# Kernel tuning notes

Hardware: AMD Instinct MI355X
Metric: run time of the kernel (lower is better)

## Reference

```python
import jax, jax.numpy as jnp
import numpy as np

B, P, M, C = 64, 8732, 16, 81
THRESHOLD = 0.5
NEG_POS_RATIO = 3
ALPHA = 1.0  # config.reg_weights
EPS = 1e-7


def cxcy_to_xy(c):
    return jnp.concatenate([c[..., :2] - c[..., 2:] / 2.0,
                            c[..., :2] + c[..., 2:] / 2.0], axis=-1)


def _rand_boxes_cxcy(key, shape):
    k1, k2 = jax.random.split(key)
    cxcy = jax.random.uniform(k1, shape + (2,), minval=0.2, maxval=0.8)
    wh = jax.random.uniform(k2, shape + (2,), minval=0.05, maxval=0.35)
    return jnp.concatenate([cxcy, wh], axis=-1)


def setup_inputs() -> dict:
    key = jax.random.key(0)
    ks = jax.random.split(key, 5)
    predicted_locs = cxcy_to_xy(_rand_boxes_cxcy(ks[0], (B, P)))          # valid corner boxes
    predicted_scores = jax.random.normal(ks[1], (B, P, C), dtype=jnp.float32)
    boxes = jnp.clip(cxcy_to_xy(_rand_boxes_cxcy(ks[2], (B, M))), 0.0, 1.0)  # GT corner boxes
    labels = jax.random.randint(ks[3], (B, M), 1, C)                       # object labels (1..C-1)
    priors_cxcy = _rand_boxes_cxcy(ks[4], (P,))
    return {"predicted_locs": predicted_locs, "predicted_scores": predicted_scores,
            "boxes": boxes, "labels": labels, "priors_cxcy": priors_cxcy}


def jaccard(a, b):
    # a: [M,4], b: [P,4] corner boxes -> [M,P] IoU
    lt = jnp.maximum(a[:, None, :2], b[None, :, :2])
    rb = jnp.minimum(a[:, None, 2:], b[None, :, 2:])
    wh = jnp.clip(rb - lt, 0.0)
    inter = wh[..., 0] * wh[..., 1]
    area_a = (a[:, 2] - a[:, 0]) * (a[:, 3] - a[:, 1])
    area_b = (b[:, 2] - b[:, 0]) * (b[:, 3] - b[:, 1])
    return inter / (area_a[:, None] + area_b[None, :] - inter)


def diou_loss(b1, b2):
    # corner boxes, elementwise over leading dims -> per-box loss 1 - DIoU
    lt = jnp.maximum(b1[..., :2], b2[..., :2])
    rb = jnp.minimum(b1[..., 2:], b2[..., 2:])
    wh = jnp.clip(rb - lt, 0.0)
    inter = wh[..., 0] * wh[..., 1]
    area1 = (b1[..., 2] - b1[..., 0]) * (b1[..., 3] - b1[..., 1])
    area2 = (b2[..., 2] - b2[..., 0]) * (b2[..., 3] - b2[..., 1])
    iou = inter / (area1 + area2 - inter + EPS)
    c1 = (b1[..., :2] + b1[..., 2:]) / 2.0
    c2 = (b2[..., :2] + b2[..., 2:]) / 2.0
    inter_diag = jnp.sum((c1 - c2) ** 2, axis=-1)
    enc_lt = jnp.minimum(b1[..., :2], b2[..., :2])
    enc_rb = jnp.maximum(b1[..., 2:], b2[..., 2:])
    outer_diag = jnp.sum((enc_rb - enc_lt) ** 2, axis=-1)
    dious = jnp.clip(iou - inter_diag / (outer_diag + EPS), -1.0, 1.0)
    return 1.0 - dious


def reference(predicted_locs, predicted_scores, boxes, labels, priors_cxcy):
    priors_xy = cxcy_to_xy(priors_cxcy)

    def assign(boxes_i, labels_i):
        overlap = jaccard(boxes_i, priors_xy)              # [M, P]
        ovl_prior = overlap.max(axis=0)                    # best overlap per prior
        obj_prior = overlap.argmax(axis=0)                 # best object per prior
        ovl_obj = overlap.max(axis=1)                      # best overlap per object
        prior_obj = overlap.argmax(axis=1)                 # best prior per object
        valid = ovl_obj > 0
        j_idx = jnp.cumsum(valid.astype(jnp.int32)) - 1    # index within filtered list (faithful)
        idx = jnp.where(valid, prior_obj, P)               # P -> dropped (out of bounds)
        ovl_prior = ovl_prior.at[idx].set(1.0, mode='drop')
        obj_prior = obj_prior.at[idx].set(j_idx, mode='drop')
        lab = labels_i[obj_prior]
        label_pos = jnp.where(ovl_prior < THRESHOLD, 0, lab)
        label_neg = jnp.where(ovl_prior < THRESHOLD - 0.1, -1, lab)
        return label_pos, label_neg

    true_classes, true_neg_classes = jax.vmap(assign)(boxes, labels)  # [B,P] each
    positive = true_classes > 0                                        # [B,P]
    pos_f = positive.astype(jnp.float32)
    n_pos_total = jnp.sum(pos_f)

    # Localization loss: DIoU(pred_pos, pred_pos) with reduce='mean' (faithful to source)
    per_box = diou_loss(predicted_locs, predicted_locs)                # [B,P]
    loc_loss = jnp.sum(per_box * pos_f) / jnp.maximum(n_pos_total, 1.0)

    # Confidence loss: per-prior CE + hard-negative mining (neg_pos_ratio)
    logp = jax.nn.log_softmax(predicted_scores, axis=-1)
    conf_all = -jnp.take_along_axis(logp, true_classes[..., None], axis=-1)[..., 0]  # [B,P]
    conf_pos_sum = jnp.sum(conf_all * pos_f)
    conf_neg = jnp.where(positive, 0.0, conf_all)
    conf_neg_sorted = -jnp.sort(-conf_neg, axis=-1)                    # descending
    n_hard = NEG_POS_RATIO * jnp.sum(positive, axis=1)                 # [B]
    hard_mask = (jnp.arange(P)[None, :] < n_hard[:, None]).astype(jnp.float32)
    conf_loss = (jnp.sum(conf_neg_sorted * hard_mask) + conf_pos_sum) / n_pos_total

    return conf_loss + ALPHA * loc_loss
```

## Files before the change

### kernel.cpp

```cpp
#include <hip/hip_runtime.h>
#include <math.h>

#define B_ 64
#define P_ 8732
#define M_ 16
#define C_ 81
#define THRESH 0.5f
#define EPS_ 1e-7f

#define CE_BLOCKS 2048
#define NBLK_CE CE_BLOCKS

__global__ __launch_bounds__(1024) void assign_kernel(
    const float* __restrict__ boxes,
    const int*   __restrict__ labels,
    const float* __restrict__ priors,
    int*         __restrict__ true_classes,
    int*         __restrict__ n_pos)
{
    const int b = blockIdx.x;
    const int tid = threadIdx.x;
    const int lane = tid & 63;
    const int wv = tid >> 6;

    __shared__ float s_ovl[P_];
    __shared__ unsigned char s_obj[P_];
    __shared__ float s_bx[M_][4];
    __shared__ float s_barea[M_];
    __shared__ int   s_lab[M_];
    __shared__ float s_wv[M_][16];
    __shared__ int   s_wp[M_][16];
    __shared__ float s_ovl_obj[M_];
    __shared__ int   s_prior_obj[M_];
    __shared__ int   s_cnt[16];

    if (tid < M_*4) ((float*)s_bx)[tid] = boxes[b*M_*4 + tid];
    if (tid < M_)   s_lab[tid] = labels[b*M_ + tid];
    __syncthreads();
    if (tid < M_)
        s_barea[tid] = (s_bx[tid][2]-s_bx[tid][0])*(s_bx[tid][3]-s_bx[tid][1]);
    __syncthreads();

    float bestv[M_]; int bestp[M_];
    #pragma unroll
    for (int m = 0; m < M_; ++m) { bestv[m] = -1.0f; bestp[m] = 0x7fffffff; }

    for (int p = tid; p < P_; p += 1024) {
        float4 pc = ((const float4*)priors)[p];
        float px1 = pc.x - pc.z*0.5f, py1 = pc.y - pc.w*0.5f;
        float px2 = pc.x + pc.z*0.5f, py2 = pc.y + pc.w*0.5f;
        float parea = (px2-px1)*(py2-py1);
        float bv = -1.0f; int bm = 0;
        #pragma unroll
        for (int m = 0; m < M_; ++m) {
            float ix1 = fmaxf(s_bx[m][0], px1);
            float iy1 = fmaxf(s_bx[m][1], py1);
            float ix2 = fminf(s_bx[m][2], px2);
            float iy2 = fminf(s_bx[m][3], py2);
            float iw = fmaxf(ix2-ix1, 0.0f);
            float ih = fmaxf(iy2-iy1, 0.0f);
            float inter = iw*ih;
            float iou = inter / (s_barea[m] + parea - inter);
            if (iou > bv) { bv = iou; bm = m; }
            if (iou > bestv[m]) { bestv[m] = iou; bestp[m] = p; }
        }
        s_ovl[p] = bv;
        s_obj[p] = (unsigned char)bm;
    }

    #pragma unroll
    for (int m = 0; m < M_; ++m) {
        float v = bestv[m]; int p = bestp[m];
        #pragma unroll
        for (int o = 32; o; o >>= 1) {
            float v2 = __shfl_xor(v, o);
            int   p2 = __shfl_xor(p, o);
            if (v2 > v || (v2 == v && p2 < p)) { v = v2; p = p2; }
        }
        if (lane == 0) { s_wv[m][wv] = v; s_wp[m][wv] = p; }
    }
    __syncthreads();

    if (tid < M_) {
        float v = s_wv[tid][0]; int p = s_wp[tid][0];
        #pragma unroll
        for (int w = 1; w < 16; ++w) {
            float v2 = s_wv[tid][w]; int p2 = s_wp[tid][w];
            if (v2 > v || (v2 == v && p2 < p)) { v = v2; p = p2; }
        }
        s_ovl_obj[tid] = v; s_prior_obj[tid] = p;
    }
    __syncthreads();

    if (tid == 0) {
        int cnt = 0;
        for (int m = 0; m < M_; ++m) {
            if (s_ovl_obj[m] > 0.0f) {
                int p = s_prior_obj[m];
                s_ovl[p] = 1.0f;
                s_obj[p] = (unsigned char)cnt;
                cnt++;
            }
        }
    }
    __syncthreads();

    int cpos = 0;
    for (int p = tid; p < P_; p += 1024) {
        int tc = 0;
        if (!(s_ovl[p] < THRESH)) tc = s_lab[s_obj[p]];
        true_classes[(size_t)b*P_ + p] = tc;
        cpos += (tc > 0);
    }
    #pragma unroll
    for (int o = 32; o; o >>= 1) cpos += __shfl_xor(cpos, o);
    if (lane == 0) s_cnt[wv] = cpos;
    __syncthreads();
    if (tid == 0) {
        int t = 0;
        #pragma unroll
        for (int w = 0; w < 16; ++w) t += s_cnt[w];
        n_pos[b] = t;
    }
}

__global__ __launch_bounds__(256) void ce_loc_kernel(
    const float* __restrict__ scores,
    const float* __restrict__ locs,
    const int*   __restrict__ tcls,
    float*       __restrict__ conf_neg,
    float*       __restrict__ blk_pos,
    float*       __restrict__ blk_loc)
{
    const int tid  = threadIdx.x;
    const int lane = tid & 63;
    const int j    = lane & 15;
    const int g    = lane >> 4;
    const int wv   = tid >> 6;
    const int gwave = blockIdx.x * 4 + wv;
    const int ngrp  = CE_BLOCKS * 4;
    const int NG = (B_ * P_) / 4;

    __shared__ float s_red[4][2];

    float p_acc = 0.f, l_acc = 0.f;

    for (int grp = gwave; grp < NG; grp += ngrp) {
        const int r = grp * 4 + g;
        const float* row = scores + (size_t)r * C_;

        float x[6];
        #pragma unroll
        for (int k = 0; k < 5; ++k) x[k] = row[16*k + j];
        x[5] = (j == 0) ? row[80] : -INFINITY;

        float mx = fmaxf(fmaxf(fmaxf(x[0], x[1]), fmaxf(x[2], x[3])),
                         fmaxf(x[4], x[5]));
        #pragma unroll
        for (int o = 1; o < 16; o <<= 1) mx = fmaxf(mx, __shfl_xor(mx, o));

        const int t = tcls[r];
        float e = 0.f, st = 0.f;
        #pragma unroll
        for (int k = 0; k < 6; ++k) {
            e += __expf(x[k] - mx);
            const int idx = 16*k + j;
            if (idx == t) st = x[k];
        }
        #pragma unroll
        for (int o = 1; o < 16; o <<= 1) {
            e  += __shfl_xor(e, o);
            st += __shfl_xor(st, o);
        }

        if (j == 0) {
            float conf = mx + __logf(e) - st;
            if (t > 0) {
                conf_neg[r] = 0.f;
                p_acc += conf;
                float4 bx = ((const float4*)locs)[r];
                float w = bx.z - bx.x, h = bx.w - bx.y;
                float iw = fmaxf(w, 0.f), ih = fmaxf(h, 0.f);
                float inter = iw * ih;
                float area  = w * h;
                float iou   = inter / (area + area - inter + EPS_);
                float diou  = fminf(fmaxf(iou, -1.f), 1.f);
                l_acc += 1.f - diou;
            } else {
                conf_neg[r] = fmaxf(conf, 0.f);
            }
        }
    }

    #pragma unroll
    for (int o = 32; o; o >>= 1) {
        p_acc += __shfl_xor(p_acc, o);
        l_acc += __shfl_xor(l_acc, o);
    }
    if (lane == 0) { s_red[wv][0] = p_acc; s_red[wv][1] = l_acc; }
    __syncthreads();
    if (tid == 0) {
        blk_pos[blockIdx.x] = s_red[0][0] + s_red[1][0] + s_red[2][0] + s_red[3][0];
        blk_loc[blockIdx.x] = s_red[0][1] + s_red[1][1] + s_red[2][1] + s_red[3][1];
    }
}

__global__ __launch_bounds__(1024) void topk_kernel(
    const float* __restrict__ conf_neg,
    const int*   __restrict__ n_pos,
    float*       __restrict__ hard)
{
    const int b = blockIdx.x;
    const int tid = threadIdx.x;
    const int lane = tid & 63;
    const int wv = tid >> 6;

    __shared__ float s_v[P_];
    __shared__ int   s_hist[16][256];
    __shared__ int   s_cg[257];
    __shared__ int   s_sel;
    __shared__ int   s_t[16];
    __shared__ float s_f[16];

    for (int i = tid; i < P_; i += 1024) s_v[i] = conf_neg[(size_t)b*P_ + i];
    int k = 3 * n_pos[b];
    if (k <= 0) { if (tid == 0) hard[b] = 0.f; return; }
    if (k > P_) k = P_;
    __syncthreads();

    const unsigned masks[4]  = {0u, 0xFF800000u, 0xFFFF8000u, 0xFFFFFF80u};
    const int      shifts[4] = {23, 15, 7, 0};

    unsigned prefix = 0u;
    int k_rem = k;

    for (int rd = 0; rd < 4; ++rd) {
        const unsigned hm = masks[rd];
        const int sh = shifts[rd];

        ((int*)s_hist)[tid] = 0;
        ((int*)s_hist)[tid + 1024] = 0;
        ((int*)s_hist)[tid + 2048] = 0;
        ((int*)s_hist)[tid + 3072] = 0;
        __syncthreads();

        for (int i = tid; i < P_; i += 1024) {
            unsigned u = __float_as_uint(s_v[i]);
            if ((u & hm) == prefix)
                atomicAdd(&s_hist[wv][(u >> sh) & 0xFF], 1);
        }
        __syncthreads();

        if (wv == 0) {
            int carry = 0;
            for (int c = 3; c >= 0; --c) {
                int bin = c * 64 + lane;
                int tot = 0;
                #pragma unroll
                for (int w = 0; w < 16; ++w) tot += s_hist[w][bin];
                #pragma unroll
                for (int o = 1; o < 64; o <<= 1) {
                    int v = __shfl_down(tot, o);
                    if (lane + o < 64) tot += v;
                }
                int cg = tot + carry;
                s_cg[bin] = cg;
                carry = __shfl(cg, 0);
            }
            if (lane == 0) s_cg[256] = 0;
        }
        __syncthreads();

        if (tid < 256) {
            if (s_cg[tid] >= k_rem && s_cg[tid + 1] < k_rem) s_sel = tid;
        }
        __syncthreads();

        const int bsel = s_sel;
        k_rem -= s_cg[bsel + 1];
        prefix |= (unsigned)bsel << sh;
        __syncthreads();
    }

    const float tval = __uint_as_float(prefix);

    float sum = 0.f; int cgt = 0;
    for (int i = tid; i < P_; i += 1024) {
        float v = s_v[i];
        if (v > tval) { sum += v; cgt++; }
    }
    #pragma unroll
    for (int o = 32; o; o >>= 1) { sum += __shfl_xor(sum, o); cgt += __shfl_xor(cgt, o); }
    if (lane == 0) { s_f[wv] = sum; s_t[wv] = cgt; }
    __syncthreads();
    if (tid == 0) {
        float s = 0.f; int c = 0;
        #pragma unroll
        for (int w = 0; w < 16; ++w) { s += s_f[w]; c += s_t[w]; }
        hard[b] = s + (float)(k - c) * tval;
    }
}

__global__ __launch_bounds__(256) void final_kernel(
    const float* __restrict__ blk_pos,
    const float* __restrict__ blk_loc,
    const float* __restrict__ hard,
    const int*   __restrict__ n_pos,
    float*       __restrict__ out)
{
    const int tid = threadIdx.x;
    const int lane = tid & 63;
    const int wv = tid >> 6;
    __shared__ double sd[4][4];

    double p = 0.0, l = 0.0, h = 0.0, np = 0.0;
    for (int i = tid; i < NBLK_CE; i += 256) { p += blk_pos[i]; l += blk_loc[i]; }
    if (tid < B_) { h = hard[tid]; np = (double)n_pos[tid]; }

    #pragma unroll
    for (int o = 32; o; o >>= 1) {
        p += __shfl_xor(p, o); l += __shfl_xor(l, o);
        h += __shfl_xor(h, o); np += __shfl_xor(np, o);
    }
    if (lane == 0) { sd[wv][0] = p; sd[wv][1] = l; sd[wv][2] = h; sd[wv][3] = np; }
    __syncthreads();
    if (tid == 0) {
        double tp = 0, tl = 0, th = 0, tn = 0;
        #pragma unroll
        for (int w = 0; w < 4; ++w) { tp += sd[w][0]; tl += sd[w][1]; th += sd[w][2]; tn += sd[w][3]; }
        double conf_loss = (th + tp) / tn;
        double loc_loss  = tl / fmax(tn, 1.0);
        out[0] = (float)(conf_loss + 1.0 * loc_loss);
    }
}

extern "C" void kernel_launch(void* const* d_in, const int* in_sizes, int n_in,
                              void* d_out, int out_size, void* d_ws, size_t ws_size,
                              hipStream_t stream) {
    const float* predicted_locs   = (const float*)d_in[0];
    const float* predicted_scores = (const float*)d_in[1];
    const float* boxes            = (const float*)d_in[2];
    const int*   labels           = (const int*)d_in[3];
    const float* priors           = (const float*)d_in[4];
    float* out = (float*)d_out;

    char* ws = (char*)d_ws;
    size_t off = 0;
    int*    true_classes = (int*)(ws + off);   off += sizeof(int)   * (size_t)B_ * P_;
    float*  conf_neg     = (float*)(ws + off); off += sizeof(float) * (size_t)B_ * P_;
    int*    n_pos        = (int*)(ws + off);   off += sizeof(int)   * B_;
    float*  hard         = (float*)(ws + off); off += sizeof(float) * B_;
    float*  blk_pos      = (float*)(ws + off); off += sizeof(float) * NBLK_CE;
    float*  blk_loc      = (float*)(ws + off); off += sizeof(float) * NBLK_CE;

    assign_kernel<<<B_, 1024, 0, stream>>>(boxes, labels, priors,
                                           true_classes, n_pos);
    ce_loc_kernel<<<CE_BLOCKS, 256, 0, stream>>>(predicted_scores, predicted_locs,
                                                 true_classes, conf_neg,
                                                 blk_pos, blk_loc);
    topk_kernel<<<B_, 1024, 0, stream>>>(conf_neg, n_pos, hard);
    final_kernel<<<1, 256, 0, stream>>>(blk_pos, blk_loc, hard, n_pos, out);
}
```

Before: 359.4 us.

## Stage CE score tiles in LDS with coalesced float4 loads, one block per tile

Rewrites the cross-entropy kernel so each block copies a contiguous 64-row tile of scores into shared memory with float4 loads, replacing the strided per-row global reads of the grid-stride loop. Four threads then handle each row from LDS, and the true-class score is read directly instead of being gathered through shuffles. The conf_neg writes are staged in shared memory and written out coalesced. The grid grows to one block per tile (8732 blocks), which adds more partial sums for the final kernel to reduce and uses more LDS per block.

```diff
diff --git a/kernel.cpp b/kernel.cpp
--- a/kernel.cpp
+++ b/kernel.cpp
@@ -8,8 +8,8 @@
 #define THRESH 0.5f
 #define EPS_ 1e-7f
 
-#define CE_BLOCKS 2048
-#define NBLK_CE CE_BLOCKS
+#define CE_TILE 64
+#define NBLK_CE ((B_ * P_) / CE_TILE)
 
 __global__ __launch_bounds__(1024) void assign_kernel(
     const float* __restrict__ boxes,
@@ -132,63 +132,67 @@
     float*       __restrict__ blk_pos,
     float*       __restrict__ blk_loc)
 {
+    __shared__ float s[CE_TILE * C_];
+    __shared__ int   s_tc[CE_TILE];
+    __shared__ float s_cf[CE_TILE];
+    __shared__ float s_red[4][2];
+
     const int tid  = threadIdx.x;
+    const int tile = blockIdx.x;
     const int lane = tid & 63;
-    const int j    = lane & 15;
-    const int g    = lane >> 4;
     const int wv   = tid >> 6;
-    const int gwave = blockIdx.x * 4 + wv;
-    const int ngrp  = CE_BLOCKS * 4;
-    const int NG = (B_ * P_) / 4;
-
-    __shared__ float s_red[4][2];
+
+    {
+        const float4* g4 = (const float4*)(scores + (size_t)tile * CE_TILE * C_);
+        float4* s4 = (float4*)s;
+        #pragma unroll
+        for (int k = 0; k < 5; ++k) s4[tid + 256*k] = g4[tid + 256*k];
+        if (tid < 1296 - 1280) s4[tid + 1280] = g4[tid + 1280];
+        if (tid < CE_TILE) s_tc[tid] = tcls[tile * CE_TILE + tid];
+    }
+    __syncthreads();
+
+    const int q    = tid & 3;
+    const int lrow = tid >> 2;
+    const float* row = s + lrow * C_;
+
+    float x[21];
+    #pragma unroll
+    for (int k = 0; k < 21; ++k) {
+        const int idx = q + 4*k;
+        x[k] = (idx < C_) ? row[idx] : -INFINITY;
+    }
+
+    float mx = x[0];
+    #pragma unroll
+    for (int k = 1; k < 21; ++k) mx = fmaxf(mx, x[k]);
+    mx = fmaxf(mx, __shfl_xor(mx, 1));
+    mx = fmaxf(mx, __shfl_xor(mx, 2));
+
+    float e = 0.f;
+    #pragma unroll
+    for (int k = 0; k < 21; ++k) e += __expf(x[k] - mx);
+    e += __shfl_xor(e, 1);
+    e += __shfl_xor(e, 2);
 
     float p_acc = 0.f, l_acc = 0.f;
-
-    for (int grp = gwave; grp < NG; grp += ngrp) {
-        const int r = grp * 4 + g;
-        const float* row = scores + (size_t)r * C_;
-
-        float x[6];
-        #pragma unroll
-        for (int k = 0; k < 5; ++k) x[k] = row[16*k + j];
-        x[5] = (j == 0) ? row[80] : -INFINITY;
-
-        float mx = fmaxf(fmaxf(fmaxf(x[0], x[1]), fmaxf(x[2], x[3])),
-                         fmaxf(x[4], x[5]));
-        #pragma unroll
-        for (int o = 1; o < 16; o <<= 1) mx = fmaxf(mx, __shfl_xor(mx, o));
-
-        const int t = tcls[r];
-        float e = 0.f, st = 0.f;
-        #pragma unroll
-        for (int k = 0; k < 6; ++k) {
-            e += __expf(x[k] - mx);
-            const int idx = 16*k + j;
-            if (idx == t) st = x[k];
-        }
-        #pragma unroll
-        for (int o = 1; o < 16; o <<= 1) {
-            e  += __shfl_xor(e, o);
-            st += __shfl_xor(st, o);
-        }
-
-        if (j == 0) {
-            float conf = mx + __logf(e) - st;
-            if (t > 0) {
-                conf_neg[r] = 0.f;
-                p_acc += conf;
-                float4 bx = ((const float4*)locs)[r];
-                float w = bx.z - bx.x, h = bx.w - bx.y;
-                float iw = fmaxf(w, 0.f), ih = fmaxf(h, 0.f);
-                float inter = iw * ih;
-                float area  = w * h;
-                float iou   = inter / (area + area - inter + EPS_);
-                float diou  = fminf(fmaxf(iou, -1.f), 1.f);
-                l_acc += 1.f - diou;
-            } else {
-                conf_neg[r] = fmaxf(conf, 0.f);
-            }
+    if (q == 0) {
+        const int r = tile * CE_TILE + lrow;
+        const int t = s_tc[lrow];
+        float conf = mx + __logf(e) - row[t];
+        if (t > 0) {
+            s_cf[lrow] = 0.f;
+            p_acc = conf;
+            float4 bx = ((const float4*)locs)[r];
+            float w = bx.z - bx.x, h = bx.w - bx.y;
+            float iw = fmaxf(w, 0.f), ih = fmaxf(h, 0.f);
+            float inter = iw * ih;
+            float area  = w * h;
+            float iou   = inter / (area + area - inter + EPS_);
+            float diou  = fminf(fmaxf(iou, -1.f), 1.f);
+            l_acc = 1.f - diou;
+        } else {
+            s_cf[lrow] = fmaxf(conf, 0.f);
         }
     }
 
@@ -199,9 +203,11 @@
     }
     if (lane == 0) { s_red[wv][0] = p_acc; s_red[wv][1] = l_acc; }
     __syncthreads();
-    if (tid == 0) {
-        blk_pos[blockIdx.x] = s_red[0][0] + s_red[1][0] + s_red[2][0] + s_red[3][0];
-        blk_loc[blockIdx.x] = s_red[0][1] + s_red[1][1] + s_red[2][1] + s_red[3][1];
+
+    if (wv == 0) conf_neg[tile * CE_TILE + lane] = s_cf[lane];
+    if (tid == 0) {
+        blk_pos[tile] = s_red[0][0] + s_red[1][0] + s_red[2][0] + s_red[3][0];
+        blk_loc[tile] = s_red[0][1] + s_red[1][1] + s_red[2][1] + s_red[3][1];
     }
 }
 
@@ -355,9 +361,9 @@
 
     assign_kernel<<<B_, 1024, 0, stream>>>(boxes, labels, priors,
                                            true_classes, n_pos);
-    ce_loc_kernel<<<CE_BLOCKS, 256, 0, stream>>>(predicted_scores, predicted_locs,
-                                                 true_classes, conf_neg,
-                                                 blk_pos, blk_loc);
+    ce_loc_kernel<<<NBLK_CE, 256, 0, stream>>>(predicted_scores, predicted_locs,
+                                               true_classes, conf_neg,
+                                               blk_pos, blk_loc);
     topk_kernel<<<B_, 1024, 0, stream>>>(conf_neg, n_pos, hard);
     final_kernel<<<1, 256, 0, stream>>>(blk_pos, blk_loc, hard, n_pos, out);
 }
```

Result: no change. 360.8 us (+0.4%).
